# Kernel optimization log

Measured on AMD Instinct MI355X. Metric: run time of the kernel, lower is better.

The kernel has to match this reference:

```python
import jax, jax.numpy as jnp
import numpy as np

D_MODEL = 1024
NUM_HEADS = 16
HEAD_DIM = D_MODEL // NUM_HEADS


def setup_inputs() -> dict:
    key = jax.random.key(0)
    ks = jax.random.split(key, 5)
    scale = 1.0 / np.sqrt(D_MODEL)
    x = jax.random.normal(ks[0], (2, 2048, D_MODEL), dtype=jnp.float32)
    W_qkv = jax.random.normal(ks[1], (D_MODEL, 3 * D_MODEL), dtype=jnp.float32) * scale
    b_qkv = jnp.zeros((3 * D_MODEL,), dtype=jnp.float32)
    W_proj = jax.random.normal(ks[2], (D_MODEL, D_MODEL), dtype=jnp.float32) * scale
    b_proj = jnp.zeros((D_MODEL,), dtype=jnp.float32)
    return {"x": x, "W_qkv": W_qkv, "b_qkv": b_qkv, "W_proj": W_proj, "b_proj": b_proj}


def reference(x, W_qkv, b_qkv, W_proj, b_proj):
    B, S, D = x.shape
    qkv = x @ W_qkv + b_qkv                      # [B,S,3D]
    qkv = qkv.reshape(B, S, 3, NUM_HEADS, HEAD_DIM)
    qkv = jnp.transpose(qkv, (2, 0, 3, 1, 4))    # [3,B,H,S,hd]
    q, k, v = qkv[0], qkv[1], qkv[2]
    scores = jnp.einsum('bhqd,bhkd->bhqk', q, k) / jnp.sqrt(jnp.asarray(HEAD_DIM, x.dtype))
    probs = jax.nn.softmax(scores, axis=-1)
    out = jnp.einsum('bhqk,bhkd->bhqd', probs, v)  # [B,H,S,hd]
    out = jnp.transpose(out, (0, 2, 1, 3)).reshape(B, S, D)
    return out @ W_proj + b_proj
```

## Files before the change

kernel.cpp:

```cpp
#include <hip/hip_runtime.h>
#include <math.h>

#define B_ 2
#define S_ 2048
#define D_ 1024
#define H_ 16
#define HD_ 64

typedef __bf16 bf16x8 __attribute__((ext_vector_type(8)));
typedef __bf16 bf16x4 __attribute__((ext_vector_type(4)));
typedef __bf16 bf16x2 __attribute__((ext_vector_type(2)));
typedef float f32x4 __attribute__((ext_vector_type(4)));
typedef float f32x16 __attribute__((ext_vector_type(16)));
typedef unsigned u32x2 __attribute__((ext_vector_type(2)));

#define GLOAD16(gsrc, ldst) \
  __builtin_amdgcn_global_load_lds((const __attribute__((address_space(1))) void*)(gsrc), \
                                   (__attribute__((address_space(3))) void*)(ldst), 16, 0, 0)

#define QSCALE 0.18033688f

static __device__ __forceinline__ unsigned pack2(float a, float b) {
    bf16x2 v; v[0] = (__bf16)a; v[1] = (__bf16)b;
    return __builtin_bit_cast(unsigned, v);
}

__global__ __launch_bounds__(256) void conv_k(
    const float* __restrict__ in, __bf16* __restrict__ out)
{
    int i = (blockIdx.x * 256 + threadIdx.x) * 8;
    float4 a = *(const float4*)(in + i);
    float4 b = *(const float4*)(in + i + 4);
    bf16x8 v;
    v[0] = (__bf16)a.x; v[1] = (__bf16)a.y; v[2] = (__bf16)a.z; v[3] = (__bf16)a.w;
    v[4] = (__bf16)b.x; v[5] = (__bf16)b.y; v[6] = (__bf16)b.z; v[7] = (__bf16)b.w;
    *(bf16x8*)(out + i) = v;
}

__global__ __launch_bounds__(256) void transpose_bf16_k(
    const float* __restrict__ in, __bf16* __restrict__ t_out, int K, int N,
    int qcols, float qs)
{
    __shared__ float t[64][65];
    const int tid = threadIdx.x;
    const int bj = blockIdx.x * 64;
    const int bi = blockIdx.y * 64;
    #pragma unroll
    for (int it = 0; it < 4; ++it) {
        int idx = (tid + it * 256) * 4;
        int r = idx >> 6, c = idx & 63;
        float4 v = *(const float4*)(in + (size_t)(bi + r) * N + bj + c);
        t[r][c] = v.x; t[r][c+1] = v.y; t[r][c+2] = v.z; t[r][c+3] = v.w;
    }
    __syncthreads();
    int j = tid & 63;
    int i0 = (tid >> 6) * 16;
    float s = (bj + j) < qcols ? qs : 1.0f;
    bf16x8 h0, h1;
    #pragma unroll
    for (int ii = 0; ii < 8; ++ii) h0[ii] = (__bf16)(t[i0 + ii][j] * s);
    #pragma unroll
    for (int ii = 0; ii < 8; ++ii) h1[ii] = (__bf16)(t[i0 + 8 + ii][j] * s);
    size_t o = (size_t)(bj + j) * K + bi + i0;
    *(bf16x8*)(t_out + o) = h0; *(bf16x8*)(t_out + o + 8) = h1;
}

template<typename OutT>
__global__ __launch_bounds__(256) void gemm_nt_k(
    const __bf16* __restrict__ A, const __bf16* __restrict__ Bt,
    const float* __restrict__ bias, OutT* __restrict__ C,
    int M, int N, int K, int qcols, float qs)
{
    constexpr int TSZ = 128 * 64;
    __shared__ __bf16 sA[TSZ];
    __shared__ __bf16 sB[TSZ];

    const int tid = threadIdx.x, w = tid >> 6, l = tid & 63;
    const int lr = l & 15, lg = l >> 4;
    const int bm = blockIdx.y * 128, bn = blockIdx.x * 128;
    const int wm = w >> 1, wn = w & 1;

    f32x4 acc[4][4] = {};

    for (int k0 = 0; k0 < K; k0 += 64) {
        __syncthreads();
        #pragma unroll
        for (int c = 0; c < 4; ++c) {
            int q = w * 4 + c;
            int r = q * 8 + (l >> 3);
            int sl = ((l & 7) ^ (r & 7)) * 8;
            GLOAD16(A + (size_t)(bm + r) * K + k0 + sl, sA + q * 512);
            GLOAD16(Bt + (size_t)(bn + r) * K + k0 + sl, sB + q * 512);
        }
        __syncthreads();
        #pragma unroll
        for (int kk = 0; kk < 2; ++kk) {
            bf16x8 ah[4], bh[4];
            #pragma unroll
            for (int i = 0; i < 4; ++i) {
                int ra = wm * 64 + i * 16 + lr;
                int sa = ((kk * 4 + lg) ^ (ra & 7)) * 8;
                ah[i] = *(const bf16x8*)(sA + ra * 64 + sa);
                int rb = wn * 64 + i * 16 + lr;
                int sb = ((kk * 4 + lg) ^ (rb & 7)) * 8;
                bh[i] = *(const bf16x8*)(sB + rb * 64 + sb);
            }
            #pragma unroll
            for (int mi = 0; mi < 4; ++mi)
                #pragma unroll
                for (int ni = 0; ni < 4; ++ni)
                    acc[mi][ni] = __builtin_amdgcn_mfma_f32_16x16x32_bf16(ah[mi], bh[ni], acc[mi][ni], 0, 0, 0);
        }
    }

    #pragma unroll
    for (int ni = 0; ni < 4; ++ni) {
        int col = bn + wn * 64 + ni * 16 + lr;
        float bv = bias[col];
        if (col < qcols) bv *= qs;
        #pragma unroll
        for (int mi = 0; mi < 4; ++mi) {
            #pragma unroll
            for (int r = 0; r < 4; ++r) {
                int row = bm + wm * 64 + mi * 16 + lg * 4 + r;
                float v = acc[mi][ni][r] + bv;
                C[(size_t)row * N + col] = (OutT)v;
            }
        }
    }
}

__global__ __launch_bounds__(512) void attn32_k(
    const __bf16* __restrict__ qkv, __bf16* __restrict__ Pout,
    float* __restrict__ Lout)
{
    __shared__ __bf16 Ks[2][2][64 * 64];
    __shared__ __bf16 Vt[2][2][64 * 64];

    const int tid = threadIdx.x, w = tid >> 6, l = tid & 63;
    const int q32 = l & 31, hi = l >> 5;
    const int bid = blockIdx.x;
    const int X = bid >> 5, hb = bid & 31;
    const int qt = X >> 1, kvh = X & 1;
    const int h = hb >> 1, b = hb & 1;
    const int q0 = qt * 256;
    const int kvbase = kvh * 1024;
    const size_t ldq = 3 * D_;
    const __bf16* Qg = qkv + (size_t)b * S_ * ldq + h * HD_;
    const __bf16* Kg = Qg + D_;
    const __bf16* Vg = Qg + 2 * D_;
    const int qg = q0 + w * 32 + q32;

    bf16x8 qf[4];
    #pragma unroll
    for (int ds = 0; ds < 4; ++ds)
        qf[ds] = *(const bf16x8*)(Qg + (size_t)qg * ldq + ds * 16 + hi * 8);

    const int krow = tid >> 3;
    const int ksl  = (tid & 7) ^ (krow & 7);
    const int vk   = tid & 63;
    const int vd0  = (tid >> 6) * 8;
    int voff[8];
    #pragma unroll
    for (int j = 0; j < 8; ++j)
        voff[j] = (vd0 + j) * 128 + (((vk >> 3) ^ j) * 16) + (vk & 7) * 2;

    f32x16 o[2] = {};
    float lsum = 0.f;
    bf16x8 vrA, vrB;

    auto stageK = [&](int lt, int set, int t) {
        GLOAD16(Kg + (size_t)(kvbase + lt * 64 + krow) * ldq + ksl * 8,
                &Ks[set][t][w * 512]);
    };
    auto loadV = [&](int lt) {
        return *(const bf16x8*)(Vg + (size_t)(kvbase + lt * 64 + vk) * ldq + vd0);
    };
    auto writeV = [&](int set, int t, const bf16x8& vr) {
        #pragma unroll
        for (int j = 0; j < 8; ++j)
            *(__bf16*)((char*)&Vt[set][t][0] + voff[j]) = vr[j];
    };

    auto computeTile = [&](int set, int t) {
        f32x16 sc[2] = {};
        __builtin_amdgcn_s_setprio(1);
        #pragma unroll
        for (int kb = 0; kb < 2; ++kb) {
            int r = kb * 32 + q32;
            #pragma unroll
            for (int ds = 0; ds < 4; ++ds) {
                int slot = (ds * 2 + hi) ^ (r & 7);
                bf16x8 kf = *(const bf16x8*)((const char*)&Ks[set][t][0] + r * 128 + slot * 16);
                sc[kb] = __builtin_amdgcn_mfma_f32_32x32x16_bf16(kf, qf[ds], sc[kb], 0, 0, 0);
            }
        }
        __builtin_amdgcn_s_setprio(0);

        float sum = 0.f;
        #pragma unroll
        for (int kb = 0; kb < 2; ++kb)
            #pragma unroll
            for (int i = 0; i < 16; ++i) {
                float pv = __builtin_amdgcn_exp2f(sc[kb][i]);
                sc[kb][i] = pv;
                sum += pv;
            }
        lsum += sum;

        bf16x8 pa[2][2];
        #pragma unroll
        for (int kb = 0; kb < 2; ++kb) {
            #pragma unroll
            for (int tl = 0; tl < 2; ++tl) {
                int base = tl * 8;
                unsigned A0 = pack2(sc[kb][base + 0], sc[kb][base + 1]);
                unsigned A1 = pack2(sc[kb][base + 2], sc[kb][base + 3]);
                unsigned B0 = pack2(sc[kb][base + 4], sc[kb][base + 5]);
                unsigned B1 = pack2(sc[kb][base + 6], sc[kb][base + 7]);
                u32x2 s0 = __builtin_amdgcn_permlane32_swap(A0, B0, false, false);
                u32x2 s1 = __builtin_amdgcn_permlane32_swap(A1, B1, false, false);
                union { unsigned u[4]; bf16x8 v; } pu;
                pu.u[0] = s0[0]; pu.u[1] = s1[0]; pu.u[2] = s0[1]; pu.u[3] = s1[1];
                pa[kb][tl] = pu.v;
            }
        }

        __builtin_amdgcn_s_setprio(1);
        #pragma unroll
        for (int db = 0; db < 2; ++db) {
            int dr = db * 32 + q32;
            #pragma unroll
            for (int tt = 0; tt < 4; ++tt) {
                int slot = (tt * 2 + hi) ^ (dr & 7);
                bf16x8 vf = *(const bf16x8*)((const char*)&Vt[set][t][0] + dr * 128 + slot * 16);
                o[db] = __builtin_amdgcn_mfma_f32_32x32x16_bf16(vf, pa[tt >> 1][tt & 1], o[db], 0, 0, 0);
            }
        }
        __builtin_amdgcn_s_setprio(0);
    };

    stageK(0, 0, 0); stageK(1, 0, 1);
    vrA = loadV(0);  vrB = loadV(1);
    writeV(0, 0, vrA); writeV(0, 1, vrB);
    __syncthreads();

    constexpr int NP = 8;
    for (int pr = 0; pr < NP; ++pr) {
        const int set = pr & 1, nset = set ^ 1;
        if (pr < NP - 1) {
            stageK(2 * pr + 2, nset, 0);
            stageK(2 * pr + 3, nset, 1);
            vrA = loadV(2 * pr + 2);
            vrB = loadV(2 * pr + 3);
        }
        computeTile(set, 0);
        computeTile(set, 1);
        if (pr < NP - 1) {
            writeV(nset, 0, vrA);
            writeV(nset, 1, vrB);
        }
        __syncthreads();
    }

    lsum += __shfl_xor(lsum, 32);
    const size_t orow = (size_t)b * S_ + qg;
    __bf16* Pb = Pout + (size_t)kvh * (4096 * 1024) + orow * D_ + h * HD_;
    #pragma unroll
    for (int db = 0; db < 2; ++db)
        #pragma unroll
        for (int rg = 0; rg < 4; ++rg) {
            int d = db * 32 + 8 * rg + 4 * hi;
            bf16x4 ov;
            #pragma unroll
            for (int i = 0; i < 4; ++i) ov[i] = (__bf16)o[db][rg * 4 + i];
            *(bf16x4*)(Pb + d) = ov;
        }
    if (hi == 0)
        Lout[(size_t)kvh * (4096 * 16) + orow * 16 + h] = lsum;
}

__global__ __launch_bounds__(256) void combine_k(
    const __bf16* __restrict__ P, const float* __restrict__ L,
    __bf16* __restrict__ attnb)
{
    int i = (blockIdx.x * 256 + threadIdx.x) * 8;
    int row = i >> 10;
    int h = (i & 1023) >> 6;
    float l0 = L[row * 16 + h];
    float l1 = L[4096 * 16 + row * 16 + h];
    float inv = 1.0f / (l0 + l1);
    bf16x8 p0 = *(const bf16x8*)(P + i);
    bf16x8 p1 = *(const bf16x8*)(P + 4096 * 1024 + i);
    bf16x8 r;
    #pragma unroll
    for (int j = 0; j < 8; ++j)
        r[j] = (__bf16)(((float)p0[j] + (float)p1[j]) * inv);
    *(bf16x8*)(attnb + i) = r;
}

extern "C" void kernel_launch(void* const* d_in, const int* in_sizes, int n_in,
                              void* d_out, int out_size, void* d_ws, size_t ws_size,
                              hipStream_t stream) {
    const float* x     = (const float*)d_in[0];
    const float* Wqkv  = (const float*)d_in[1];
    const float* bqkv  = (const float*)d_in[2];
    const float* Wproj = (const float*)d_in[3];
    const float* bproj = (const float*)d_in[4];

    __bf16* ws = (__bf16*)d_ws;
    const size_t MB = 524288;
    __bf16* wp_t  = ws;
    __bf16* qkv   = ws + 2 * MB;
    __bf16* attnb = ws + 26 * MB;
    __bf16* x_bf  = ws + 34 * MB;
    __bf16* wq_t  = ws + 42 * MB;
    __bf16* Pp    = ws + 34 * MB;
    float*  Lp    = (float*)(ws + 50 * MB);

    const int M = B_ * S_;

    conv_k<<<2048, 256, 0, stream>>>(x, x_bf);
    transpose_bf16_k<<<dim3(48, 16), 256, 0, stream>>>(Wqkv, wq_t, D_, 3 * D_, D_, QSCALE);
    transpose_bf16_k<<<dim3(16, 16), 256, 0, stream>>>(Wproj, wp_t, D_, D_, 0, 1.0f);

    gemm_nt_k<__bf16><<<dim3(24, 32), 256, 0, stream>>>(
        x_bf, wq_t, bqkv, qkv, M, 3 * D_, D_, D_, QSCALE);

    attn32_k<<<512, 512, 0, stream>>>(qkv, Pp, Lp);

    combine_k<<<2048, 256, 0, stream>>>(Pp, Lp, attnb);

    gemm_nt_k<float><<<dim3(8, 32), 256, 0, stream>>>(
        attnb, wp_t, bproj, (float*)d_out, M, D_, D_, 0, 1.0f);
}
```

Baseline: 140.9 us.

## Interleave QK and PV MFMAs across tile pair and fuse prep kernels

Merges the x conversion and two weight-transpose kernels into one prep launch, dispatched by block index, to cut launch overhead and tail gaps. In the attention kernel, the two KV tiles per stage are processed together: the QK^T MFMAs for the second tile are interleaved with the PV MFMAs of the first tile, so softmax/pack work and LDS reads overlap with matrix ops. Two separate row-sum accumulators keep the dependency chains independent. This raises register pressure, since two score tiles and packed operands are live at once.

```diff
diff --git a/kernel.cpp b/kernel.cpp
--- a/kernel.cpp
+++ b/kernel.cpp
@@ -25,26 +25,36 @@
     return __builtin_bit_cast(unsigned, v);
 }
 
-__global__ __launch_bounds__(256) void conv_k(
-    const float* __restrict__ in, __bf16* __restrict__ out)
-{
-    int i = (blockIdx.x * 256 + threadIdx.x) * 8;
-    float4 a = *(const float4*)(in + i);
-    float4 b = *(const float4*)(in + i + 4);
-    bf16x8 v;
-    v[0] = (__bf16)a.x; v[1] = (__bf16)a.y; v[2] = (__bf16)a.z; v[3] = (__bf16)a.w;
-    v[4] = (__bf16)b.x; v[5] = (__bf16)b.y; v[6] = (__bf16)b.z; v[7] = (__bf16)b.w;
-    *(bf16x8*)(out + i) = v;
-}
-
-__global__ __launch_bounds__(256) void transpose_bf16_k(
-    const float* __restrict__ in, __bf16* __restrict__ t_out, int K, int N,
-    int qcols, float qs)
+__global__ __launch_bounds__(256) void prep_k(
+    const float* __restrict__ x, __bf16* __restrict__ x_bf,
+    const float* __restrict__ Wqkv, __bf16* __restrict__ wq_t,
+    const float* __restrict__ Wproj, __bf16* __restrict__ wp_t)
 {
     __shared__ float t[64][65];
     const int tid = threadIdx.x;
-    const int bj = blockIdx.x * 64;
-    const int bi = blockIdx.y * 64;
+    const int bid = blockIdx.x;
+
+    if (bid < 2048) {
+        int i = (bid * 256 + tid) * 8;
+        float4 a = *(const float4*)(x + i);
+        float4 b = *(const float4*)(x + i + 4);
+        bf16x8 v;
+        v[0] = (__bf16)a.x; v[1] = (__bf16)a.y; v[2] = (__bf16)a.z; v[3] = (__bf16)a.w;
+        v[4] = (__bf16)b.x; v[5] = (__bf16)b.y; v[6] = (__bf16)b.z; v[7] = (__bf16)b.w;
+        *(bf16x8*)(x_bf + i) = v;
+        return;
+    }
+
+    const float* in; __bf16* outp; int K, N, qcols; float qs; int bx, by;
+    if (bid < 2816) {
+        int tt = bid - 2048; bx = tt % 48; by = tt / 48;
+        in = Wqkv; outp = wq_t; K = D_; N = 3 * D_; qcols = D_; qs = QSCALE;
+    } else {
+        int tt = bid - 2816; bx = tt % 16; by = tt / 16;
+        in = Wproj; outp = wp_t; K = D_; N = D_; qcols = 0; qs = 1.0f;
+    }
+    const int bj = bx * 64;
+    const int bi = by * 64;
     #pragma unroll
     for (int it = 0; it < 4; ++it) {
         int idx = (tid + it * 256) * 4;
@@ -62,7 +72,7 @@
     #pragma unroll
     for (int ii = 0; ii < 8; ++ii) h1[ii] = (__bf16)(t[i0 + 8 + ii][j] * s);
     size_t o = (size_t)(bj + j) * K + bi + i0;
-    *(bf16x8*)(t_out + o) = h0; *(bf16x8*)(t_out + o + 8) = h1;
+    *(bf16x8*)(outp + o) = h0; *(bf16x8*)(outp + o + 8) = h1;
 }
 
 template<typename OutT>
@@ -166,7 +176,7 @@
         voff[j] = (vd0 + j) * 128 + (((vk >> 3) ^ j) * 16) + (vk & 7) * 2;
 
     f32x16 o[2] = {};
-    float lsum = 0.f;
+    float lsumA = 0.f, lsumB = 0.f;
     bf16x8 vrA, vrB;
 
     auto stageK = [&](int lt, int set, int t) {
@@ -182,21 +192,7 @@
             *(__bf16*)((char*)&Vt[set][t][0] + voff[j]) = vr[j];
     };
 
-    auto computeTile = [&](int set, int t) {
-        f32x16 sc[2] = {};
-        __builtin_amdgcn_s_setprio(1);
-        #pragma unroll
-        for (int kb = 0; kb < 2; ++kb) {
-            int r = kb * 32 + q32;
-            #pragma unroll
-            for (int ds = 0; ds < 4; ++ds) {
-                int slot = (ds * 2 + hi) ^ (r & 7);
-                bf16x8 kf = *(const bf16x8*)((const char*)&Ks[set][t][0] + r * 128 + slot * 16);
-                sc[kb] = __builtin_amdgcn_mfma_f32_32x32x16_bf16(kf, qf[ds], sc[kb], 0, 0, 0);
-            }
-        }
-        __builtin_amdgcn_s_setprio(0);
-
+    auto smPack = [&](f32x16 sc[2], bf16x8 pa[2][2], float& ls) {
         float sum = 0.f;
         #pragma unroll
         for (int kb = 0; kb < 2; ++kb)
@@ -206,11 +202,9 @@
                 sc[kb][i] = pv;
                 sum += pv;
             }
-        lsum += sum;
-
-        bf16x8 pa[2][2];
-        #pragma unroll
-        for (int kb = 0; kb < 2; ++kb) {
+        ls += sum;
+        #pragma unroll
+        for (int kb = 0; kb < 2; ++kb)
             #pragma unroll
             for (int tl = 0; tl < 2; ++tl) {
                 int base = tl * 8;
@@ -224,7 +218,59 @@
                 pu.u[0] = s0[0]; pu.u[1] = s1[0]; pu.u[2] = s0[1]; pu.u[3] = s1[1];
                 pa[kb][tl] = pu.v;
             }
-        }
+    };
+
+    auto computePair = [&](int set) {
+        f32x16 sc0[2] = {};
+        __builtin_amdgcn_s_setprio(1);
+        #pragma unroll
+        for (int kb = 0; kb < 2; ++kb) {
+            int r = kb * 32 + q32;
+            #pragma unroll
+            for (int ds = 0; ds < 4; ++ds) {
+                int slot = (ds * 2 + hi) ^ (r & 7);
+                bf16x8 kf = *(const bf16x8*)((const char*)&Ks[set][0][0] + r * 128 + slot * 16);
+                sc0[kb] = __builtin_amdgcn_mfma_f32_32x32x16_bf16(kf, qf[ds], sc0[kb], 0, 0, 0);
+            }
+        }
+        __builtin_amdgcn_s_setprio(0);
+
+        bf16x8 pa0[2][2];
+        smPack(sc0, pa0, lsumA);
+
+        f32x16 sc1[2] = {};
+        __builtin_amdgcn_s_setprio(1);
+        #pragma unroll
+        for (int st = 0; st < 4; ++st) {
+            {
+                int r = q32;
+                int slot = (st * 2 + hi) ^ (r & 7);
+                bf16x8 kf = *(const bf16x8*)((const char*)&Ks[set][1][0] + r * 128 + slot * 16);
+                sc1[0] = __builtin_amdgcn_mfma_f32_32x32x16_bf16(kf, qf[st], sc1[0], 0, 0, 0);
+            }
+            {
+                int dr = q32;
+                int slot = (st * 2 + hi) ^ (dr & 7);
+                bf16x8 vf = *(const bf16x8*)((const char*)&Vt[set][0][0] + dr * 128 + slot * 16);
+                o[0] = __builtin_amdgcn_mfma_f32_32x32x16_bf16(vf, pa0[st >> 1][st & 1], o[0], 0, 0, 0);
+            }
+            {
+                int r = 32 + q32;
+                int slot = (st * 2 + hi) ^ (r & 7);
+                bf16x8 kf = *(const bf16x8*)((const char*)&Ks[set][1][0] + r * 128 + slot * 16);
+                sc1[1] = __builtin_amdgcn_mfma_f32_32x32x16_bf16(kf, qf[st], sc1[1], 0, 0, 0);
+            }
+            {
+                int dr = 32 + q32;
+                int slot = (st * 2 + hi) ^ (dr & 7);
+                bf16x8 vf = *(const bf16x8*)((const char*)&Vt[set][0][0] + dr * 128 + slot * 16);
+                o[1] = __builtin_amdgcn_mfma_f32_32x32x16_bf16(vf, pa0[st >> 1][st & 1], o[1], 0, 0, 0);
+            }
+        }
+        __builtin_amdgcn_s_setprio(0);
+
+        bf16x8 pa1[2][2];
+        smPack(sc1, pa1, lsumB);
 
         __builtin_amdgcn_s_setprio(1);
         #pragma unroll
@@ -233,8 +279,8 @@
             #pragma unroll
             for (int tt = 0; tt < 4; ++tt) {
                 int slot = (tt * 2 + hi) ^ (dr & 7);
-                bf16x8 vf = *(const bf16x8*)((const char*)&Vt[set][t][0] + dr * 128 + slot * 16);
-                o[db] = __builtin_amdgcn_mfma_f32_32x32x16_bf16(vf, pa[tt >> 1][tt & 1], o[db], 0, 0, 0);
+                bf16x8 vf = *(const bf16x8*)((const char*)&Vt[set][1][0] + dr * 128 + slot * 16);
+                o[db] = __builtin_amdgcn_mfma_f32_32x32x16_bf16(vf, pa1[tt >> 1][tt & 1], o[db], 0, 0, 0);
             }
         }
         __builtin_amdgcn_s_setprio(0);
@@ -254,8 +300,7 @@
             vrA = loadV(2 * pr + 2);
             vrB = loadV(2 * pr + 3);
         }
-        computeTile(set, 0);
-        computeTile(set, 1);
+        computePair(set);
         if (pr < NP - 1) {
             writeV(nset, 0, vrA);
             writeV(nset, 1, vrB);
@@ -263,6 +308,7 @@
         __syncthreads();
     }
 
+    float lsum = lsumA + lsumB;
     lsum += __shfl_xor(lsum, 32);
     const size_t orow = (size_t)b * S_ + qg;
     __bf16* Pb = Pout + (size_t)kvh * (4096 * 1024) + orow * D_ + h * HD_;
@@ -320,9 +366,7 @@
 
     const int M = B_ * S_;
 
-    conv_k<<<2048, 256, 0, stream>>>(x, x_bf);
-    transpose_bf16_k<<<dim3(48, 16), 256, 0, stream>>>(Wqkv, wq_t, D_, 3 * D_, D_, QSCALE);
-    transpose_bf16_k<<<dim3(16, 16), 256, 0, stream>>>(Wproj, wp_t, D_, D_, 0, 1.0f);
+    prep_k<<<3072, 256, 0, stream>>>(x, x_bf, Wqkv, wq_t, Wproj, wp_t);
 
     gemm_nt_k<__bf16><<<dim3(24, 32), 256, 0, stream>>>(
         x_bf, wq_t, bqkv, qkv, M, 3 * D_, D_, D_, QSCALE);
```

Result: faster. 136.3 us (-3.3%).
